# Performance work log

Measured on AMD Instinct MI355X. Metric: run time of the kernel, lower is better.

Reference implementation:

```python
import jax, jax.numpy as jnp
import numpy as np

TIME_STEPS = 20
THRESHOLD = 1.0
DECAY = 0.9


def setup_inputs() -> dict:
    key = jax.random.key(0)
    x = jax.random.uniform(key, (64, 8192), dtype=jnp.float32)
    return {"x": x}


def reference(x):
    # LIF recurrence over TIME_STEPS: mem = decay*mem + x; spike = mem >= thr;
    # record (spike, mem); then mem -= spike*thr. Sequential -> lax.scan.
    thr = jnp.asarray(THRESHOLD, dtype=x.dtype)
    decay = jnp.asarray(DECAY, dtype=x.dtype)

    def step(mem, _):
        mem = decay * mem + x
        spikes = (mem >= thr).astype(x.dtype)
        mem_out = mem  # recorded before reset
        mem_next = mem - spikes * thr
        return mem_next, (spikes, mem_out)

    mem0 = jnp.zeros_like(x)
    _, (spike_trains, membrane_potentials) = jax.lax.scan(
        step, mem0, None, length=TIME_STEPS)
    # shapes: [T, batch, features]
    return spike_trains, membrane_potentials
```

## Files before the change

kernel.cpp:

```cpp
#include <hip/hip_runtime.h>


#define TSTEPS 20

typedef float v4f __attribute__((ext_vector_type(4)));

__global__ __launch_bounds__(256) void
TemporalEncoding_57672820850797_kernel(const v4f* __restrict__ x,
                                       float* __restrict__ out, int n4) {
    int i = blockIdx.x * blockDim.x + threadIdx.x;
    if (i >= n4) return;

    const v4f xv = __builtin_nontemporal_load(&x[i]);
    v4f* __restrict__ spikes = reinterpret_cast<v4f*>(out) + i;
    v4f* __restrict__ mems   = reinterpret_cast<v4f*>(out) + (size_t)TSTEPS * n4 + i;

    float m0 = 0.f, m1 = 0.f, m2 = 0.f, m3 = 0.f;

#pragma unroll
    for (int t = 0; t < TSTEPS; ++t) {
        m0 = __fadd_rn(__fmul_rn(0.9f, m0), xv.x);
        m1 = __fadd_rn(__fmul_rn(0.9f, m1), xv.y);
        m2 = __fadd_rn(__fmul_rn(0.9f, m2), xv.z);
        m3 = __fadd_rn(__fmul_rn(0.9f, m3), xv.w);

        float s0 = (m0 >= 1.0f) ? 1.0f : 0.0f;
        float s1 = (m1 >= 1.0f) ? 1.0f : 0.0f;
        float s2 = (m2 >= 1.0f) ? 1.0f : 0.0f;
        float s3 = (m3 >= 1.0f) ? 1.0f : 0.0f;

        v4f sv; sv.x = s0; sv.y = s1; sv.z = s2; sv.w = s3;
        v4f mv; mv.x = m0; mv.y = m1; mv.z = m2; mv.w = m3;
        __builtin_nontemporal_store(sv, spikes);
        __builtin_nontemporal_store(mv, mems);
        spikes += n4;
        mems   += n4;

        m0 -= s0;
        m1 -= s1;
        m2 -= s2;
        m3 -= s3;
    }
}

extern "C" void kernel_launch(void* const* d_in, const int* in_sizes, int n_in,
                              void* d_out, int out_size, void* d_ws, size_t ws_size,
                              hipStream_t stream) {
    const float* x = (const float*)d_in[0];
    float* out = (float*)d_out;
    const int n = in_sizes[0];
    const int n4 = n / 4;
    const int block = 256;
    const int grid = (n4 + block - 1) / block;
    TemporalEncoding_57672820850797_kernel<<<grid, block, 0, stream>>>(
        (const v4f*)x, out, n4);
}
```

Before: 90.24 us.

## Split time steps across grid.y groups with recompute of prefix state

Adds a second grid dimension that splits the 20 time steps into 4 groups. Each block recomputes the membrane recurrence up to its group's starting step without storing anything, then writes only its 5 steps. This gives four times as many blocks (512 → 2048) to raise parallelism and memory-level concurrency for a store-bound kernel. The cost is redundant arithmetic, reading x once per group, and dropping the nontemporal load hint.

Result: no change. 91.66 us (+1.6%).

```diff
diff --git a/kernel.cpp b/kernel.cpp
--- a/kernel.cpp
+++ b/kernel.cpp
@@ -2,6 +2,8 @@
 
 
 #define TSTEPS 20
+#define GROUPS 4
+#define SPG (TSTEPS / GROUPS)
 
 typedef float v4f __attribute__((ext_vector_type(4)));
 
@@ -10,24 +12,39 @@
                                        float* __restrict__ out, int n4) {
     int i = blockIdx.x * blockDim.x + threadIdx.x;
     if (i >= n4) return;
+    const int tstart = blockIdx.y * SPG;
 
-    const v4f xv = __builtin_nontemporal_load(&x[i]);
-    v4f* __restrict__ spikes = reinterpret_cast<v4f*>(out) + i;
-    v4f* __restrict__ mems   = reinterpret_cast<v4f*>(out) + (size_t)TSTEPS * n4 + i;
+    const v4f xv = x[i];
 
     float m0 = 0.f, m1 = 0.f, m2 = 0.f, m3 = 0.f;
 
+#define LIF_STEP(S0, S1, S2, S3)                       \
+    m0 = __fadd_rn(__fmul_rn(0.9f, m0), xv.x);         \
+    m1 = __fadd_rn(__fmul_rn(0.9f, m1), xv.y);         \
+    m2 = __fadd_rn(__fmul_rn(0.9f, m2), xv.z);         \
+    m3 = __fadd_rn(__fmul_rn(0.9f, m3), xv.w);         \
+    S0 = (m0 >= 1.0f) ? 1.0f : 0.0f;                   \
+    S1 = (m1 >= 1.0f) ? 1.0f : 0.0f;                   \
+    S2 = (m2 >= 1.0f) ? 1.0f : 0.0f;                   \
+    S3 = (m3 >= 1.0f) ? 1.0f : 0.0f;
+
+    for (int t = 0; t < tstart; ++t) {
+        float s0, s1, s2, s3;
+        LIF_STEP(s0, s1, s2, s3)
+        m0 -= s0;
+        m1 -= s1;
+        m2 -= s2;
+        m3 -= s3;
+    }
+
+    v4f* __restrict__ spikes =
+        reinterpret_cast<v4f*>(out) + (size_t)tstart * n4 + i;
+    v4f* __restrict__ mems = spikes + (size_t)TSTEPS * n4;
+
 #pragma unroll
-    for (int t = 0; t < TSTEPS; ++t) {
-        m0 = __fadd_rn(__fmul_rn(0.9f, m0), xv.x);
-        m1 = __fadd_rn(__fmul_rn(0.9f, m1), xv.y);
-        m2 = __fadd_rn(__fmul_rn(0.9f, m2), xv.z);
-        m3 = __fadd_rn(__fmul_rn(0.9f, m3), xv.w);
-
-        float s0 = (m0 >= 1.0f) ? 1.0f : 0.0f;
-        float s1 = (m1 >= 1.0f) ? 1.0f : 0.0f;
-        float s2 = (m2 >= 1.0f) ? 1.0f : 0.0f;
-        float s3 = (m3 >= 1.0f) ? 1.0f : 0.0f;
+    for (int k = 0; k < SPG; ++k) {
+        float s0, s1, s2, s3;
+        LIF_STEP(s0, s1, s2, s3)
 
         v4f sv; sv.x = s0; sv.y = s1; sv.z = s2; sv.w = s3;
         v4f mv; mv.x = m0; mv.y = m1; mv.z = m2; mv.w = m3;
@@ -41,6 +58,7 @@
         m2 -= s2;
         m3 -= s3;
     }
+#undef LIF_STEP
 }
 
 extern "C" void kernel_launch(void* const* d_in, const int* in_sizes, int n_in,
@@ -51,7 +69,7 @@
     const int n = in_sizes[0];
     const int n4 = n / 4;
     const int block = 256;
-    const int grid = (n4 + block - 1) / block;
+    dim3 grid((n4 + block - 1) / block, GROUPS);
     TemporalEncoding_57672820850797_kernel<<<grid, block, 0, stream>>>(
         (const v4f*)x, out, n4);
 }
```
